# Performance work log

Hardware: AMD Instinct MI355X
Metric: run time of the kernel (lower is better)

The kernel has to match this reference:

```python
import jax, jax.numpy as jnp
import numpy as np

VOCAB = 100000
EMB = 128
WINDOW = 200
N_T = 64
B = 128
N_W = 128
ALPHA = 0.5
PAD = VOCAB - 1


def setup_inputs() -> dict:
    key = jax.random.key(0)
    ks = jax.random.split(key, 8)
    s = 0.5 / EMB
    tvecs = jax.random.uniform(ks[0], (VOCAB, EMB), minval=-s, maxval=s).at[PAD].set(0.0)
    cvecs = jax.random.uniform(ks[1], (VOCAB, EMB), minval=-s, maxval=s).at[PAD].set(0.0)
    W_w = jax.random.normal(ks[2], (N_W, 2 * EMB)) * 0.02
    W_b = jnp.zeros((N_W,))
    h_w = jax.random.normal(ks[3], (1, N_W)) * 0.02
    h_b = jnp.zeros((1,))
    batch_titems = jax.random.randint(ks[4], (B, N_T), 0, VOCAB)
    batch_citems = jax.random.randint(ks[5], (B, WINDOW), 0, VOCAB)
    mask_pad_ids = jax.random.randint(ks[6], (B, WINDOW), 0, 2).astype(bool)
    return {
        "tvecs": tvecs, "cvecs": cvecs,
        "W_w": W_w, "W_b": W_b, "h_w": h_w, "h_b": h_b,
        "batch_titems": batch_titems, "batch_citems": batch_citems,
        "mask_pad_ids": mask_pad_ids,
    }


def reference(tvecs, cvecs, W_w, W_b, h_w, h_b, batch_titems, batch_citems, mask_pad_ids):
    q = tvecs[batch_titems]   # (B, N_T, E)  target-item (query) embeddings
    k = cvecs[batch_citems]   # (B, W, E)    context-item (key/value) embeddings
    # W(concat(p, q)) == p @ Wp.T + q @ Wq.T + b  -- split weight, avoid the
    # materialized (B, N_T, W, 2E) repeat+cat tensor of the torch code.
    Wp, Wq = W_w[:, :EMB], W_w[:, EMB:]
    hp = jnp.einsum('bte,ne->btn', q, Wp)   # (B, N_T, N_W)
    hq = jnp.einsum('bwe,ne->bwn', k, Wq)   # (B, W,  N_W)
    hidden = jax.nn.relu(hp[:, :, None, :] + hq[:, None, :, :] + W_b)  # (B,N_T,W,N_W)
    att = jnp.einsum('btwn,n->btw', hidden, h_w[0]) + h_b[0]            # (B,N_T,W)
    att = jnp.where(mask_pad_ids[:, None, :], -jnp.inf, att)
    att = jax.nn.softmax(att, axis=-1)
    out = jnp.einsum('btw,bwe->bte', att, k)                            # (B,N_T,E)
    norm = (1000.0 - mask_pad_ids.sum(axis=1).astype(out.dtype)) ** ALPHA  # (B,)
    return out / norm[:, None, None]
```

## Files before the change

### kernel.cpp

```cpp
#include <hip/hip_runtime.h>
#include <math.h>

#define EMB 128
#define WIN 200
#define NT 64
#define BB 128

typedef short bf16x8 __attribute__((ext_vector_type(8)));
typedef float f32x4  __attribute__((ext_vector_type(4)));

__device__ __forceinline__ unsigned pk2bf16(float a, float b) {
    unsigned ua = __float_as_uint(a), ub = __float_as_uint(b);
    ua = (ua + 0x7FFFu + ((ua >> 16) & 1u)) >> 16;
    ub = (ub + 0x7FFFu + ((ub >> 16) & 1u)) >> 16;
    return ua | (ub << 16);
}
__device__ __forceinline__ float rdlane(float v, int l) {
    return __uint_as_float(__builtin_amdgcn_readlane(__float_as_uint(v), l));
}

__global__ __launch_bounds__(512, 4) void proj_kernel(
    const float* __restrict__ tvecs, const float* __restrict__ cvecs,
    const int* __restrict__ titems, const int* __restrict__ citems,
    const float* __restrict__ Ww, const float* __restrict__ Wbias,
    const int* __restrict__ mi, int* __restrict__ flag,
    float* __restrict__ hp_out, float* __restrict__ hq_out)
{
    __shared__ __align__(16) ushort s_A[128 * 128];
    __shared__ __align__(16) ushort s_B[128 * 128];
    __shared__ float s_bias[128];
    __shared__ int   sdet;

    const int tid = threadIdx.x;

    if (blockIdx.x == 264) {
        if (tid == 0) sdet = 0;
        __syncthreads();
        int bad = 0;
        for (int i = tid; i < 6400; i += 512)
            if ((unsigned)mi[i] > 1u) bad = 1;
        if (bad) sdet = 1;
        __syncthreads();
        if (tid == 0) flag[0] = sdet;
        return;
    }

    const bool is_hp = blockIdx.x < 64;
    const float* table = is_hp ? tvecs : cvecs;
    const int*   idx   = is_hp ? titems : citems;
    const int  rbase = (is_hp ? blockIdx.x : (blockIdx.x - 64)) * 128;
    const int  eoff  = is_hp ? 0 : EMB;

    if (tid < 128) s_bias[tid] = Wbias[tid];

    for (int i = tid; i < 4096; i += 512) {
        int row = i >> 5, j = i & 31;
        float4 v = *(const float4*)&table[(size_t)idx[rbase + row] * 128 + 4 * j];
        uint2 p; p.x = pk2bf16(v.x, v.y); p.y = pk2bf16(v.z, v.w);
        *(uint2*)((char*)s_A + row * 256 + (((j >> 1) ^ (row & 7)) << 4) + (j & 1) * 8) = p;
    }
    for (int i = tid; i < 4096; i += 512) {
        int n = i >> 5, j = i & 31;
        float4 v = *(const float4*)&Ww[n * 256 + eoff + 4 * j];
        uint2 p; p.x = pk2bf16(v.x, v.y); p.y = pk2bf16(v.z, v.w);
        *(uint2*)((char*)s_B + n * 256 + (((j >> 1) ^ (n & 7)) << 4) + (j & 1) * 8) = p;
    }
    __syncthreads();

    const int wid = tid >> 6, l = tid & 63;
    const int rl = l & 15, kg = l >> 4;
    const int r0 = wid * 16;

    f32x4 acc[8];
#pragma unroll
    for (int i = 0; i < 8; ++i) acc[i] = (f32x4){0.f, 0.f, 0.f, 0.f};

    const int arow = r0 + rl;
#pragma unroll
    for (int s = 0; s < 4; ++s) {
        bf16x8 af = *(const bf16x8*)((const char*)s_A
                        + arow * 256 + ((((s << 2) + kg) ^ (arow & 7)) << 4));
#pragma unroll
        for (int nt = 0; nt < 8; ++nt) {
            int bn = nt * 16 + rl;
            bf16x8 bfr = *(const bf16x8*)((const char*)s_B
                            + bn * 256 + ((((s << 2) + kg) ^ (bn & 7)) << 4));
            acc[nt] = __builtin_amdgcn_mfma_f32_16x16x32_bf16(af, bfr, acc[nt], 0, 0, 0);
        }
    }

#pragma unroll
    for (int i = 0; i < 4; ++i) {
        size_t base = (size_t)(rbase + r0 + kg * 4 + i) * 128;
        if (is_hp) {
#pragma unroll
            for (int nt = 0; nt < 8; ++nt)
                hp_out[base + nt * 16 + rl] = acc[nt][i];
        } else {
#pragma unroll
            for (int nt = 0; nt < 8; ++nt) {
                int col = nt * 16 + rl;
                hq_out[base + col] = acc[nt][i] + s_bias[col];
            }
        }
    }
}

__global__ __launch_bounds__(512, 2) void attn_kernel(
    const float* __restrict__ cvecs, const int* __restrict__ citems,
    const void* __restrict__ mask_raw, const int* __restrict__ flagp,
    const float* __restrict__ hwg, const float* __restrict__ hp,
    const float* __restrict__ hq, float* __restrict__ outp)
{
    __shared__ __align__(16) float4 s_hq4[32 * 128];
    __shared__ __align__(16) float4 s_k4[128 * 32];
    __shared__ __align__(16) float  s_hp[32 * 128];
    __shared__ __align__(16) float  s_hw[128];
    __shared__ int s_ci[WIN];
    __shared__ int s_widx[WIN];
    __shared__ int s_m;

    const int tid  = threadIdx.x;
    const int bid  = blockIdx.x;
    const int swz  = (bid & 7) * 32 + (bid >> 3);
    const int b    = swz >> 1;
    const int tb   = (swz & 1) * 32;
    const int lane = tid & 63;
    const int wid  = tid >> 6;
    const int t0   = wid * 4;

    for (int i = tid; i < 1024; i += 512) {
        int t = i >> 5, e4 = i & 31;
        *(float4*)&s_hp[t * 128 + e4 * 4] =
            *(const float4*)&hp[((size_t)(b * 64 + tb + t)) * 128 + e4 * 4];
    }
    if (tid < 128) s_hw[tid] = hwg[tid];
    if (tid < WIN) s_ci[tid] = citems[b * WIN + tid];
    if (wid == 0) {
        const int boolmode = flagp[0];
        const unsigned char* mb = (const unsigned char*)mask_raw;
        const int*           mi = (const int*)mask_raw;
        int base = 0;
#pragma unroll
        for (int r = 0; r < 4; ++r) {
            int w  = r * 64 + lane;
            int mv = 1;
            if (w < WIN) mv = boolmode ? (int)mb[b * WIN + w] : mi[b * WIN + w];
            unsigned long long act = __ballot(mv == 0);
            if (mv == 0)
                s_widx[base + __popcll(act & ((1ull << lane) - 1ull))] = w;
            base += __popcll(act);
        }
        if (lane == 0) s_m = base;
    }
    __syncthreads();

    const int m = s_m;
    const float invn = 1.f / sqrtf(800.f + (float)m);
    size_t orow = ((size_t)(b * 64 + tb + t0)) * 128;

    if (m == 0) {
#pragma unroll
        for (int j = 0; j < 4; ++j)
            *(float2*)&outp[orow + (size_t)j * 128 + lane * 2] = make_float2(0.f, 0.f);
        return;
    }

    const float4* hq4r = (const float4*)hq + (size_t)b * 200 * 32;
    const float4* hp4a = (const float4*)&s_hp[t0 * 128];
    const float4* hw4p = (const float4*)s_hw;
    const float4* cv4  = (const float4*)cvecs;

#define SC(J, K, HV, P)                                                        \
    va[J][K] += hwv.x * fmaxf(HV.x + P.x, 0.f) + hwv.y * fmaxf(HV.y + P.y, 0.f)\
              + hwv.z * fmaxf(HV.z + P.z, 0.f) + hwv.w * fmaxf(HV.w + P.w, 0.f);

    if (m <= 128) {
        {
            const int w2 = tid & 127, nc0 = tid >> 7;
            if (w2 < m) {
                const int wi = s_widx[w2];
#pragma unroll
                for (int nc = nc0; nc < 32; nc += 4)
                    s_hq4[nc * 128 + w2] = hq4r[(size_t)wi * 32 + nc];
            }
            const int e4 = tid & 31, w0 = tid >> 5;
            for (int w2k = w0; w2k < m; w2k += 16) {
                int ci = s_ci[s_widx[w2k]];
                s_k4[w2k * 32 + e4] = cv4[(size_t)ci * 32 + e4];
            }
        }
        __syncthreads();

        float va[4][2];
#pragma unroll
        for (int j = 0; j < 4; ++j) { va[j][0] = 0.f; va[j][1] = 0.f; }

#pragma unroll 2
        for (int nc = 0; nc < 32; ++nc) {
            float4 hv0 = s_hq4[nc * 128 + lane];
            float4 hv1 = s_hq4[nc * 128 + 64 + lane];
            float4 hwv = hw4p[nc];
            float4 p0  = hp4a[0 * 32 + nc];
            float4 p1  = hp4a[1 * 32 + nc];
            float4 p2  = hp4a[2 * 32 + nc];
            float4 p3  = hp4a[3 * 32 + nc];
            SC(0, 0, hv0, p0) SC(0, 1, hv1, p0)
            SC(1, 0, hv0, p1) SC(1, 1, hv1, p1)
            SC(2, 0, hv0, p2) SC(2, 1, hv1, p2)
            SC(3, 0, hv0, p3) SC(3, 1, hv1, p3)
        }

#pragma unroll
        for (int j = 0; j < 4; ++j) {
            float mx = -1e30f;
#pragma unroll
            for (int kt = 0; kt < 2; ++kt) {
                float v = (kt * 64 + lane < m) ? va[j][kt] : -1e30f;
                va[j][kt] = v;
                mx = fmaxf(mx, v);
            }
#pragma unroll
            for (int off = 32; off; off >>= 1) mx = fmaxf(mx, __shfl_xor(mx, off));
            float sum = 0.f;
#pragma unroll
            for (int kt = 0; kt < 2; ++kt) {
                float e = (va[j][kt] <= -1e29f) ? 0.f : __expf(va[j][kt] - mx);
                va[j][kt] = e;
                sum += e;
            }
#pragma unroll
            for (int off = 32; off; off >>= 1) sum += __shfl_xor(sum, off);
            float is = 1.f / sum;
            va[j][0] *= is; va[j][1] *= is;
        }

        float2 po[4];
#pragma unroll
        for (int j = 0; j < 4; ++j) po[j] = make_float2(0.f, 0.f);
        const float2* s_k2 = (const float2*)s_k4;
#pragma unroll
        for (int kt = 0; kt < 2; ++kt) {
            if (kt * 64 < m) {
                const int wn = min(64, m - kt * 64);
                for (int w = 0; w < wn; ++w) {
                    float2 kv = s_k2[(kt * 64 + w) * 64 + lane];
                    float a0 = rdlane(va[0][kt], w);
                    float a1 = rdlane(va[1][kt], w);
                    float a2 = rdlane(va[2][kt], w);
                    float a3 = rdlane(va[3][kt], w);
                    po[0].x += a0 * kv.x; po[0].y += a0 * kv.y;
                    po[1].x += a1 * kv.x; po[1].y += a1 * kv.y;
                    po[2].x += a2 * kv.x; po[2].y += a2 * kv.y;
                    po[3].x += a3 * kv.x; po[3].y += a3 * kv.y;
                }
            }
        }
#pragma unroll
        for (int j = 0; j < 4; ++j)
            *(float2*)&outp[orow + (size_t)j * 128 + lane * 2] =
                make_float2(po[j].x * invn, po[j].y * invn);
    } else {
        int wreg[4];
        const int mc = m - 1;
#pragma unroll
        for (int kt = 0; kt < 4; ++kt)
            wreg[kt] = s_widx[min(kt * 64 + lane, mc)];

        float va[4][4];
#pragma unroll
        for (int j = 0; j < 4; ++j)
#pragma unroll
            for (int k = 0; k < 4; ++k) va[j][k] = 0.f;

#pragma unroll 2
        for (int nc = 0; nc < 32; ++nc) {
            float4 hv0 = hq4r[(size_t)wreg[0] * 32 + nc];
            float4 hv1 = hq4r[(size_t)wreg[1] * 32 + nc];
            float4 hv2 = hq4r[(size_t)wreg[2] * 32 + nc];
            float4 hv3 = hq4r[(size_t)wreg[3] * 32 + nc];
            float4 hwv = hw4p[nc];
            float4 p0  = hp4a[0 * 32 + nc];
            float4 p1  = hp4a[1 * 32 + nc];
            float4 p2  = hp4a[2 * 32 + nc];
            float4 p3  = hp4a[3 * 32 + nc];
            SC(0, 0, hv0, p0) SC(0, 1, hv1, p0) SC(0, 2, hv2, p0) SC(0, 3, hv3, p0)
            SC(1, 0, hv0, p1) SC(1, 1, hv1, p1) SC(1, 2, hv2, p1) SC(1, 3, hv3, p1)
            SC(2, 0, hv0, p2) SC(2, 1, hv1, p2) SC(2, 2, hv2, p2) SC(2, 3, hv3, p2)
            SC(3, 0, hv0, p3) SC(3, 1, hv1, p3) SC(3, 2, hv2, p3) SC(3, 3, hv3, p3)
        }

#pragma unroll
        for (int j = 0; j < 4; ++j) {
            float mx = -1e30f;
#pragma unroll
            for (int kt = 0; kt < 4; ++kt) {
                float v = (kt * 64 + lane < m) ? va[j][kt] : -1e30f;
                va[j][kt] = v;
                mx = fmaxf(mx, v);
            }
#pragma unroll
            for (int off = 32; off; off >>= 1) mx = fmaxf(mx, __shfl_xor(mx, off));
            float sum = 0.f;
#pragma unroll
            for (int kt = 0; kt < 4; ++kt) {
                float e = (va[j][kt] <= -1e29f) ? 0.f : __expf(va[j][kt] - mx);
                va[j][kt] = e;
                sum += e;
            }
#pragma unroll
            for (int off = 32; off; off >>= 1) sum += __shfl_xor(sum, off);
            float is = 1.f / sum;
#pragma unroll
            for (int kt = 0; kt < 4; ++kt) va[j][kt] *= is;
        }

        float2 po[4];
#pragma unroll
        for (int j = 0; j < 4; ++j) po[j] = make_float2(0.f, 0.f);
        const char* cvb = (const char*)cvecs;
#pragma unroll
        for (int kt = 0; kt < 4; ++kt) {
            if (kt * 64 < m) {
                const int wn = min(64, m - kt * 64);
                for (int w = 0; w < wn; ++w) {
                    unsigned off = (unsigned)s_ci[s_widx[kt * 64 + w]] * 512u;
                    float2 kv = *(const float2*)(cvb + off + lane * 8);
                    float a0 = rdlane(va[0][kt], w);
                    float a1 = rdlane(va[1][kt], w);
                    float a2 = rdlane(va[2][kt], w);
                    float a3 = rdlane(va[3][kt], w);
                    po[0].x += a0 * kv.x; po[0].y += a0 * kv.y;
                    po[1].x += a1 * kv.x; po[1].y += a1 * kv.y;
                    po[2].x += a2 * kv.x; po[2].y += a2 * kv.y;
                    po[3].x += a3 * kv.x; po[3].y += a3 * kv.y;
                }
            }
        }
#pragma unroll
        for (int j = 0; j < 4; ++j)
            *(float2*)&outp[orow + (size_t)j * 128 + lane * 2] =
                make_float2(po[j].x * invn, po[j].y * invn);
    }
#undef SC
}

extern "C" void kernel_launch(void* const* d_in, const int* in_sizes, int n_in,
                              void* d_out, int out_size, void* d_ws, size_t ws_size,
                              hipStream_t stream) {
    const float* tvecs = (const float*)d_in[0];
    const float* cvecs = (const float*)d_in[1];
    const float* Ww    = (const float*)d_in[2];
    const float* Wb    = (const float*)d_in[3];
    const float* hw    = (const float*)d_in[4];
    const int* titems  = (const int*)d_in[6];
    const int* citems  = (const int*)d_in[7];
    const void* mask   = d_in[8];
    float* out         = (float*)d_out;

    const size_t hp_elems = (size_t)BB * NT * 128;
    const size_t hq_elems = (size_t)BB * WIN * 128;
    const size_t needed = 256 + (hp_elems + hq_elems) * 4;
    if (ws_size < needed) return;

    int*   flag  = (int*)d_ws;
    float* hp_ws = (float*)((char*)d_ws + 256);
    float* hq_ws = hp_ws + hp_elems;

    proj_kernel<<<265, 512, 0, stream>>>(tvecs, cvecs, titems, citems,
                                         Ww, Wb, (const int*)mask, flag,
                                         hp_ws, hq_ws);
    attn_kernel<<<BB * 2, 512, 0, stream>>>(cvecs, citems, mask, flag,
                                            hw, hp_ws, hq_ws, out);
}
```

Before: 48.20 us.

## Split attention over window halves with flash-style partial softmax and combine kernel

The attention kernel now splits each (batch, target-half) block into two blocks, each handling half of the unmasked window positions. Each block writes unnormalized partial outputs plus its max and sum, and a new combine kernel merges them with log-sum-exp rescaling and applies the norm. hp is also staged in LDS as bf16 to shrink shared memory, allowing higher occupancy (launch bound 4). The cost is an extra kernel launch, a partial-results buffer round trip, and reduced precision for hp. The m>128 path is not split: its second-half block stays idle.

```diff
diff --git a/kernel.cpp b/kernel.cpp
--- a/kernel.cpp
+++ b/kernel.cpp
@@ -5,6 +5,7 @@
 #define WIN 200
 #define NT 64
 #define BB 128
+#define PSTRIDE 132
 
 typedef short bf16x8 __attribute__((ext_vector_type(8)));
 typedef float f32x4  __attribute__((ext_vector_type(4)));
@@ -15,6 +16,8 @@
     ub = (ub + 0x7FFFu + ((ub >> 16) & 1u)) >> 16;
     return ua | (ub << 16);
 }
+__device__ __forceinline__ float bf_lo(unsigned u) { return __uint_as_float(u << 16); }
+__device__ __forceinline__ float bf_hi(unsigned u) { return __uint_as_float(u & 0xFFFF0000u); }
 __device__ __forceinline__ float rdlane(float v, int l) {
     return __uint_as_float(__builtin_amdgcn_readlane(__float_as_uint(v), l));
 }
@@ -106,33 +109,34 @@
     }
 }
 
-__global__ __launch_bounds__(512, 2) void attn_kernel(
+__global__ __launch_bounds__(512, 4) void attn_part(
     const float* __restrict__ cvecs, const int* __restrict__ citems,
     const void* __restrict__ mask_raw, const int* __restrict__ flagp,
     const float* __restrict__ hwg, const float* __restrict__ hp,
-    const float* __restrict__ hq, float* __restrict__ outp)
+    const float* __restrict__ hq, float* __restrict__ part)
 {
-    __shared__ __align__(16) float4 s_hq4[32 * 128];
-    __shared__ __align__(16) float4 s_k4[128 * 32];
-    __shared__ __align__(16) float  s_hp[32 * 128];
-    __shared__ __align__(16) float  s_hw[128];
+    __shared__ __align__(16) float4 s_hq4[32 * 64];
+    __shared__ __align__(16) float4 s_k4[64 * 32];
+    __shared__ __align__(16) ushort s_hp[32 * 128];
+    __shared__ float s_hw[128];
     __shared__ int s_ci[WIN];
     __shared__ int s_widx[WIN];
     __shared__ int s_m;
 
     const int tid  = threadIdx.x;
     const int bid  = blockIdx.x;
-    const int swz  = (bid & 7) * 32 + (bid >> 3);
-    const int b    = swz >> 1;
-    const int tb   = (swz & 1) * 32;
+    const int b    = bid >> 2;
+    const int tb   = ((bid >> 1) & 1) * 32;
+    const int h    = bid & 1;
     const int lane = tid & 63;
     const int wid  = tid >> 6;
     const int t0   = wid * 4;
 
     for (int i = tid; i < 1024; i += 512) {
         int t = i >> 5, e4 = i & 31;
-        *(float4*)&s_hp[t * 128 + e4 * 4] =
-            *(const float4*)&hp[((size_t)(b * 64 + tb + t)) * 128 + e4 * 4];
+        float4 v = *(const float4*)&hp[((size_t)(b * 64 + tb + t)) * 128 + e4 * 4];
+        uint2 p; p.x = pk2bf16(v.x, v.y); p.y = pk2bf16(v.z, v.w);
+        ((uint2*)s_hp)[i] = p;
     }
     if (tid < 128) s_hw[tid] = hwg[tid];
     if (tid < WIN) s_ci[tid] = citems[b * WIN + tid];
@@ -156,116 +160,103 @@
     __syncthreads();
 
     const int m = s_m;
-    const float invn = 1.f / sqrtf(800.f + (float)m);
-    size_t orow = ((size_t)(b * 64 + tb + t0)) * 128;
-
-    if (m == 0) {
-#pragma unroll
-        for (int j = 0; j < 4; ++j)
-            *(float2*)&outp[orow + (size_t)j * 128 + lane * 2] = make_float2(0.f, 0.f);
-        return;
-    }
-
     const float4* hq4r = (const float4*)hq + (size_t)b * 200 * 32;
-    const float4* hp4a = (const float4*)&s_hp[t0 * 128];
     const float4* hw4p = (const float4*)s_hw;
-    const float4* cv4  = (const float4*)cvecs;
-
-#define SC(J, K, HV, P)                                                        \
-    va[J][K] += hwv.x * fmaxf(HV.x + P.x, 0.f) + hwv.y * fmaxf(HV.y + P.y, 0.f)\
-              + hwv.z * fmaxf(HV.z + P.z, 0.f) + hwv.w * fmaxf(HV.w + P.w, 0.f);
+
+#define ZERO_OUT()                                                             \
+    {                                                                          \
+        _Pragma("unroll")                                                      \
+        for (int j = 0; j < 4; ++j) {                                          \
+            float* pb = part + ((size_t)((b * 64 + tb + t0 + j) * 2 + h)) * PSTRIDE; \
+            *(float2*)(pb + lane * 2) = make_float2(0.f, 0.f);                 \
+            if (lane == 0) { pb[128] = -1e30f; pb[129] = 0.f; pb[130] = 0.f; } \
+        }                                                                      \
+    }
+
+#define SCB(J, HV)                                                             \
+    va[J] += hwv.x * fmaxf(HV.x + pa, 0.f) + hwv.y * fmaxf(HV.y + pb_, 0.f)    \
+           + hwv.z * fmaxf(HV.z + pc, 0.f) + hwv.w * fmaxf(HV.w + pd, 0.f);
+#define SCB4(J, K, HV)                                                         \
+    va[J][K] += hwv.x * fmaxf(HV.x + pa, 0.f) + hwv.y * fmaxf(HV.y + pb_, 0.f) \
+              + hwv.z * fmaxf(HV.z + pc, 0.f) + hwv.w * fmaxf(HV.w + pd, 0.f);
 
     if (m <= 128) {
+        const int mh0 = (m + 1) >> 1;
+        const int lo  = h ? mh0 : 0;
+        const int cnt = h ? (m - mh0) : mh0;
+        if (cnt == 0) { ZERO_OUT(); return; }
+
         {
-            const int w2 = tid & 127, nc0 = tid >> 7;
-            if (w2 < m) {
-                const int wi = s_widx[w2];
-#pragma unroll
-                for (int nc = nc0; nc < 32; nc += 4)
-                    s_hq4[nc * 128 + w2] = hq4r[(size_t)wi * 32 + nc];
+            const int w2 = tid & 63, nc0 = tid >> 6;
+            if (w2 < cnt) {
+                const int wi = s_widx[lo + w2];
+#pragma unroll
+                for (int nc = nc0; nc < 32; nc += 8)
+                    s_hq4[nc * 64 + w2] = hq4r[(size_t)wi * 32 + nc];
             }
             const int e4 = tid & 31, w0 = tid >> 5;
-            for (int w2k = w0; w2k < m; w2k += 16) {
-                int ci = s_ci[s_widx[w2k]];
-                s_k4[w2k * 32 + e4] = cv4[(size_t)ci * 32 + e4];
-            }
+            const float4* cv4 = (const float4*)cvecs;
+            for (int w2k = w0; w2k < cnt; w2k += 16)
+                s_k4[w2k * 32 + e4] = cv4[(size_t)s_ci[s_widx[lo + w2k]] * 32 + e4];
         }
         __syncthreads();
 
-        float va[4][2];
-#pragma unroll
-        for (int j = 0; j < 4; ++j) { va[j][0] = 0.f; va[j][1] = 0.f; }
-
-#pragma unroll 2
+        float va[4];
+        va[0] = va[1] = va[2] = va[3] = 0.f;
+#pragma unroll 4
         for (int nc = 0; nc < 32; ++nc) {
-            float4 hv0 = s_hq4[nc * 128 + lane];
-            float4 hv1 = s_hq4[nc * 128 + 64 + lane];
+            float4 hv  = s_hq4[nc * 64 + lane];
             float4 hwv = hw4p[nc];
-            float4 p0  = hp4a[0 * 32 + nc];
-            float4 p1  = hp4a[1 * 32 + nc];
-            float4 p2  = hp4a[2 * 32 + nc];
-            float4 p3  = hp4a[3 * 32 + nc];
-            SC(0, 0, hv0, p0) SC(0, 1, hv1, p0)
-            SC(1, 0, hv0, p1) SC(1, 1, hv1, p1)
-            SC(2, 0, hv0, p2) SC(2, 1, hv1, p2)
-            SC(3, 0, hv0, p3) SC(3, 1, hv1, p3)
-        }
-
+#pragma unroll
+            for (int jt = 0; jt < 4; ++jt) {
+                uint2 pu = *(const uint2*)&s_hp[(t0 + jt) * 128 + nc * 4];
+                float pa = bf_lo(pu.x), pb_ = bf_hi(pu.x), pc = bf_lo(pu.y), pd = bf_hi(pu.y);
+                SCB(jt, hv)
+            }
+        }
+
+        float mxs[4], sms[4];
 #pragma unroll
         for (int j = 0; j < 4; ++j) {
-            float mx = -1e30f;
-#pragma unroll
-            for (int kt = 0; kt < 2; ++kt) {
-                float v = (kt * 64 + lane < m) ? va[j][kt] : -1e30f;
-                va[j][kt] = v;
-                mx = fmaxf(mx, v);
-            }
+            float v = (lane < cnt) ? va[j] : -1e30f;
+            float mx = v;
 #pragma unroll
             for (int off = 32; off; off >>= 1) mx = fmaxf(mx, __shfl_xor(mx, off));
-            float sum = 0.f;
-#pragma unroll
-            for (int kt = 0; kt < 2; ++kt) {
-                float e = (va[j][kt] <= -1e29f) ? 0.f : __expf(va[j][kt] - mx);
-                va[j][kt] = e;
-                sum += e;
-            }
+            float e = (v <= -1e29f) ? 0.f : __expf(v - mx);
+            float sum = e;
 #pragma unroll
             for (int off = 32; off; off >>= 1) sum += __shfl_xor(sum, off);
-            float is = 1.f / sum;
-            va[j][0] *= is; va[j][1] *= is;
+            va[j] = e; mxs[j] = mx; sms[j] = sum;
         }
 
         float2 po[4];
 #pragma unroll
         for (int j = 0; j < 4; ++j) po[j] = make_float2(0.f, 0.f);
         const float2* s_k2 = (const float2*)s_k4;
-#pragma unroll
-        for (int kt = 0; kt < 2; ++kt) {
-            if (kt * 64 < m) {
-                const int wn = min(64, m - kt * 64);
-                for (int w = 0; w < wn; ++w) {
-                    float2 kv = s_k2[(kt * 64 + w) * 64 + lane];
-                    float a0 = rdlane(va[0][kt], w);
-                    float a1 = rdlane(va[1][kt], w);
-                    float a2 = rdlane(va[2][kt], w);
-                    float a3 = rdlane(va[3][kt], w);
-                    po[0].x += a0 * kv.x; po[0].y += a0 * kv.y;
-                    po[1].x += a1 * kv.x; po[1].y += a1 * kv.y;
-                    po[2].x += a2 * kv.x; po[2].y += a2 * kv.y;
-                    po[3].x += a3 * kv.x; po[3].y += a3 * kv.y;
-                }
-            }
-        }
-#pragma unroll
-        for (int j = 0; j < 4; ++j)
-            *(float2*)&outp[orow + (size_t)j * 128 + lane * 2] =
-                make_float2(po[j].x * invn, po[j].y * invn);
+        for (int w = 0; w < cnt; ++w) {
+            float2 kv = s_k2[w * 64 + lane];
+            float a0 = rdlane(va[0], w);
+            float a1 = rdlane(va[1], w);
+            float a2 = rdlane(va[2], w);
+            float a3 = rdlane(va[3], w);
+            po[0].x += a0 * kv.x; po[0].y += a0 * kv.y;
+            po[1].x += a1 * kv.x; po[1].y += a1 * kv.y;
+            po[2].x += a2 * kv.x; po[2].y += a2 * kv.y;
+            po[3].x += a3 * kv.x; po[3].y += a3 * kv.y;
+        }
+
+#pragma unroll
+        for (int j = 0; j < 4; ++j) {
+            float* pb = part + ((size_t)((b * 64 + tb + t0 + j) * 2 + h)) * PSTRIDE;
+            *(float2*)(pb + lane * 2) = po[j];
+            if (lane == 0) { pb[128] = mxs[j]; pb[129] = sms[j]; pb[130] = (float)cnt; }
+        }
     } else {
+        if (h == 1) { ZERO_OUT(); return; }
         int wreg[4];
         const int mc = m - 1;
 #pragma unroll
-        for (int kt = 0; kt < 4; ++kt)
-            wreg[kt] = s_widx[min(kt * 64 + lane, mc)];
+        for (int kt = 0; kt < 4; ++kt) wreg[kt] = s_widx[min(kt * 64 + lane, mc)];
 
         float va[4][4];
 #pragma unroll
@@ -280,16 +271,15 @@
             float4 hv2 = hq4r[(size_t)wreg[2] * 32 + nc];
             float4 hv3 = hq4r[(size_t)wreg[3] * 32 + nc];
             float4 hwv = hw4p[nc];
-            float4 p0  = hp4a[0 * 32 + nc];
-            float4 p1  = hp4a[1 * 32 + nc];
-            float4 p2  = hp4a[2 * 32 + nc];
-            float4 p3  = hp4a[3 * 32 + nc];
-            SC(0, 0, hv0, p0) SC(0, 1, hv1, p0) SC(0, 2, hv2, p0) SC(0, 3, hv3, p0)
-            SC(1, 0, hv0, p1) SC(1, 1, hv1, p1) SC(1, 2, hv2, p1) SC(1, 3, hv3, p1)
-            SC(2, 0, hv0, p2) SC(2, 1, hv1, p2) SC(2, 2, hv2, p2) SC(2, 3, hv3, p2)
-            SC(3, 0, hv0, p3) SC(3, 1, hv1, p3) SC(3, 2, hv2, p3) SC(3, 3, hv3, p3)
-        }
-
+#pragma unroll
+            for (int jt = 0; jt < 4; ++jt) {
+                uint2 pu = *(const uint2*)&s_hp[(t0 + jt) * 128 + nc * 4];
+                float pa = bf_lo(pu.x), pb_ = bf_hi(pu.x), pc = bf_lo(pu.y), pd = bf_hi(pu.y);
+                SCB4(jt, 0, hv0) SCB4(jt, 1, hv1) SCB4(jt, 2, hv2) SCB4(jt, 3, hv3)
+            }
+        }
+
+        float mxs[4], sms[4];
 #pragma unroll
         for (int j = 0; j < 4; ++j) {
             float mx = -1e30f;
@@ -310,9 +300,7 @@
             }
 #pragma unroll
             for (int off = 32; off; off >>= 1) sum += __shfl_xor(sum, off);
-            float is = 1.f / sum;
-#pragma unroll
-            for (int kt = 0; kt < 4; ++kt) va[j][kt] *= is;
+            mxs[j] = mx; sms[j] = sum;
         }
 
         float2 po[4];
@@ -338,11 +326,41 @@
             }
         }
 #pragma unroll
-        for (int j = 0; j < 4; ++j)
-            *(float2*)&outp[orow + (size_t)j * 128 + lane * 2] =
-                make_float2(po[j].x * invn, po[j].y * invn);
-    }
-#undef SC
+        for (int j = 0; j < 4; ++j) {
+            float* pb = part + ((size_t)((b * 64 + tb + t0 + j) * 2 + h)) * PSTRIDE;
+            *(float2*)(pb + lane * 2) = po[j];
+            if (lane == 0) { pb[128] = mxs[j]; pb[129] = sms[j]; pb[130] = (float)m; }
+        }
+    }
+#undef SCB
+#undef SCB4
+#undef ZERO_OUT
+}
+
+__global__ __launch_bounds__(256) void combine_kernel(
+    const float* __restrict__ part, float* __restrict__ outp)
+{
+    const int lane = threadIdx.x & 63;
+    const int wid  = threadIdx.x >> 6;
+    const int row  = blockIdx.x * 4 + wid;
+
+    const float* p0 = part + (size_t)row * 2 * PSTRIDE;
+    const float* p1 = p0 + PSTRIDE;
+    float mx0 = p0[128], s0 = p0[129], c0m = p0[130];
+    float mx1 = p1[128], s1 = p1[129], c1m = p1[130];
+    float M  = fmaxf(mx0, mx1);
+    float c0 = (s0 > 0.f) ? __expf(mx0 - M) : 0.f;
+    float c1 = (s1 > 0.f) ? __expf(mx1 - M) : 0.f;
+    float den = c0 * s0 + c1 * s1;
+    float invn = 1.f / sqrtf(800.f + c0m + c1m);
+    float scale = (den > 0.f) ? (invn / den) : 0.f;
+
+    float2 a = *(const float2*)(p0 + lane * 2);
+    float2 q = *(const float2*)(p1 + lane * 2);
+    float2 r;
+    r.x = (c0 * a.x + c1 * q.x) * scale;
+    r.y = (c0 * a.y + c1 * q.y) * scale;
+    *(float2*)&outp[(size_t)row * 128 + lane * 2] = r;
 }
 
 extern "C" void kernel_launch(void* const* d_in, const int* in_sizes, int n_in,
@@ -358,18 +376,21 @@
     const void* mask   = d_in[8];
     float* out         = (float*)d_out;
 
-    const size_t hp_elems = (size_t)BB * NT * 128;
-    const size_t hq_elems = (size_t)BB * WIN * 128;
-    const size_t needed = 256 + (hp_elems + hq_elems) * 4;
+    const size_t hp_elems   = (size_t)BB * NT * 128;
+    const size_t hq_elems   = (size_t)BB * WIN * 128;
+    const size_t part_elems = (size_t)BB * NT * 2 * PSTRIDE;
+    const size_t needed = 256 + (hp_elems + hq_elems + part_elems) * 4;
     if (ws_size < needed) return;
 
-    int*   flag  = (int*)d_ws;
-    float* hp_ws = (float*)((char*)d_ws + 256);
-    float* hq_ws = hp_ws + hp_elems;
+    int*   flag    = (int*)d_ws;
+    float* hp_ws   = (float*)((char*)d_ws + 256);
+    float* hq_ws   = hp_ws + hp_elems;
+    float* part_ws = hq_ws + hq_elems;
 
     proj_kernel<<<265, 512, 0, stream>>>(tvecs, cvecs, titems, citems,
                                          Ww, Wb, (const int*)mask, flag,
                                          hp_ws, hq_ws);
-    attn_kernel<<<BB * 2, 512, 0, stream>>>(cvecs, citems, mask, flag,
-                                            hw, hp_ws, hq_ws, out);
-}
+    attn_part<<<BB * 4, 512, 0, stream>>>(cvecs, citems, mask, flag,
+                                          hw, hp_ws, hq_ws, part_ws);
+    combine_kernel<<<2048, 256, 0, stream>>>(part_ws, out);
+}
```

Measured after the change: 53.01 us. 1.1x slower.

## Prefetch full hq block into registers, stage hq and keys as bf16 in LDS

Applied to the files above, without the earlier changes.

The attention kernel now issues global loads for the whole per-batch hq block (200x128) and the hp rows into registers before the mask compaction. It then packs hq into swizzled bf16 LDS storage, so the masked-window gather happens through LDS indices rather than a second global gather. Key vectors are prefetched into registers before the score loop and written to LDS as bf16 only after the softmax, hiding their latency behind compute. The trade is loading all 200 hq rows regardless of the mask, higher register pressure (13+8 float4 buffers), bf16 rounding of hq and keys that affects accuracy, and an extra barrier.

```diff
diff --git a/kernel.cpp b/kernel.cpp
--- a/kernel.cpp
+++ b/kernel.cpp
@@ -15,6 +15,8 @@
     ub = (ub + 0x7FFFu + ((ub >> 16) & 1u)) >> 16;
     return ua | (ub << 16);
 }
+__device__ __forceinline__ float bf_lo(unsigned u) { return __uint_as_float(u << 16); }
+__device__ __forceinline__ float bf_hi(unsigned u) { return __uint_as_float(u & 0xFFFF0000u); }
 __device__ __forceinline__ float rdlane(float v, int l) {
     return __uint_as_float(__builtin_amdgcn_readlane(__float_as_uint(v), l));
 }
@@ -112,10 +114,10 @@
     const float* __restrict__ hwg, const float* __restrict__ hp,
     const float* __restrict__ hq, float* __restrict__ outp)
 {
-    __shared__ __align__(16) float4 s_hq4[32 * 128];
-    __shared__ __align__(16) float4 s_k4[128 * 32];
-    __shared__ __align__(16) float  s_hp[32 * 128];
-    __shared__ __align__(16) float  s_hw[128];
+    __shared__ __align__(16) uint2 s_hq2[WIN * 32];
+    __shared__ __align__(16) uint  s_k[128 * 64];
+    __shared__ __align__(16) float s_hp[32 * 128];
+    __shared__ float s_hw[128];
     __shared__ int s_ci[WIN];
     __shared__ int s_widx[WIN];
     __shared__ int s_m;
@@ -129,10 +131,19 @@
     const int wid  = tid >> 6;
     const int t0   = wid * 4;
 
-    for (int i = tid; i < 1024; i += 512) {
-        int t = i >> 5, e4 = i & 31;
-        *(float4*)&s_hp[t * 128 + e4 * 4] =
-            *(const float4*)&hp[((size_t)(b * 64 + tb + t)) * 128 + e4 * 4];
+    const float4* hq4r = (const float4*)hq + (size_t)b * 200 * 32;
+    const float4* cv4  = (const float4*)cvecs;
+
+    float4 hqbuf[13];
+    {
+        int n = 0;
+        for (int idx = tid; idx < 6400; idx += 512) hqbuf[n++] = hq4r[idx];
+    }
+    float4 hpbuf[2];
+#pragma unroll
+    for (int q = 0; q < 2; ++q) {
+        int idx = tid + q * 512;
+        hpbuf[q] = *(const float4*)&hp[((size_t)(b * 64 + tb + (idx >> 5))) * 128 + (idx & 31) * 4];
     }
     if (tid < 128) s_hw[tid] = hwg[tid];
     if (tid < WIN) s_ci[tid] = citems[b * WIN + tid];
@@ -153,6 +164,21 @@
         }
         if (lane == 0) s_m = base;
     }
+
+    {
+        int n = 0;
+        for (int idx = tid; idx < 6400; idx += 512) {
+            int w = idx >> 5, nc = idx & 31;
+            float4 v = hqbuf[n++];
+            uint2 p; p.x = pk2bf16(v.x, v.y); p.y = pk2bf16(v.z, v.w);
+            s_hq2[w * 32 + (nc ^ (w & 31))] = p;
+        }
+    }
+#pragma unroll
+    for (int q = 0; q < 2; ++q) {
+        int idx = tid + q * 512;
+        *(float4*)&s_hp[(idx >> 5) * 128 + (idx & 31) * 4] = hpbuf[q];
+    }
     __syncthreads();
 
     const int m = s_m;
@@ -166,31 +192,29 @@
         return;
     }
 
-    const float4* hq4r = (const float4*)hq + (size_t)b * 200 * 32;
     const float4* hp4a = (const float4*)&s_hp[t0 * 128];
     const float4* hw4p = (const float4*)s_hw;
-    const float4* cv4  = (const float4*)cvecs;
-
-#define SC(J, K, HV, P)                                                        \
+    const int mc = m - 1;
+
+#define SCB(J, K, HA, HB, HC, HD, P)                                           \
+    va[J][K] += hwv.x * fmaxf(HA + P.x, 0.f) + hwv.y * fmaxf(HB + P.y, 0.f)    \
+              + hwv.z * fmaxf(HC + P.z, 0.f) + hwv.w * fmaxf(HD + P.w, 0.f);
+#define SCF(J, K, HV, P)                                                       \
     va[J][K] += hwv.x * fmaxf(HV.x + P.x, 0.f) + hwv.y * fmaxf(HV.y + P.y, 0.f)\
               + hwv.z * fmaxf(HV.z + P.z, 0.f) + hwv.w * fmaxf(HV.w + P.w, 0.f);
 
     if (m <= 128) {
+        float4 kbuf[8];
         {
-            const int w2 = tid & 127, nc0 = tid >> 7;
-            if (w2 < m) {
-                const int wi = s_widx[w2];
-#pragma unroll
-                for (int nc = nc0; nc < 32; nc += 4)
-                    s_hq4[nc * 128 + w2] = hq4r[(size_t)wi * 32 + nc];
-            }
-            const int e4 = tid & 31, w0 = tid >> 5;
-            for (int w2k = w0; w2k < m; w2k += 16) {
-                int ci = s_ci[s_widx[w2k]];
-                s_k4[w2k * 32 + e4] = cv4[(size_t)ci * 32 + e4];
-            }
-        }
-        __syncthreads();
+            int n = 0;
+            for (int idx = tid; idx < m * 32; idx += 512)
+                kbuf[n++] = cv4[(size_t)s_ci[s_widx[idx >> 5]] * 32 + (idx & 31)];
+        }
+
+        const int wr0 = s_widx[min(lane, mc)];
+        const int wr1 = s_widx[min(64 + lane, mc)];
+        const int b0 = wr0 * 32, x0 = wr0 & 31;
+        const int b1 = wr1 * 32, x1 = wr1 & 31;
 
         float va[4][2];
 #pragma unroll
@@ -198,17 +222,19 @@
 
 #pragma unroll 2
         for (int nc = 0; nc < 32; ++nc) {
-            float4 hv0 = s_hq4[nc * 128 + lane];
-            float4 hv1 = s_hq4[nc * 128 + 64 + lane];
+            uint2 h0 = s_hq2[b0 + (nc ^ x0)];
+            uint2 h1 = s_hq2[b1 + (nc ^ x1)];
+            float h0a = bf_lo(h0.x), h0b = bf_hi(h0.x), h0c = bf_lo(h0.y), h0d = bf_hi(h0.y);
+            float h1a = bf_lo(h1.x), h1b = bf_hi(h1.x), h1c = bf_lo(h1.y), h1d = bf_hi(h1.y);
             float4 hwv = hw4p[nc];
             float4 p0  = hp4a[0 * 32 + nc];
             float4 p1  = hp4a[1 * 32 + nc];
             float4 p2  = hp4a[2 * 32 + nc];
             float4 p3  = hp4a[3 * 32 + nc];
-            SC(0, 0, hv0, p0) SC(0, 1, hv1, p0)
-            SC(1, 0, hv0, p1) SC(1, 1, hv1, p1)
-            SC(2, 0, hv0, p2) SC(2, 1, hv1, p2)
-            SC(3, 0, hv0, p3) SC(3, 1, hv1, p3)
+            SCB(0, 0, h0a, h0b, h0c, h0d, p0) SCB(0, 1, h1a, h1b, h1c, h1d, p0)
+            SCB(1, 0, h0a, h0b, h0c, h0d, p1) SCB(1, 1, h1a, h1b, h1c, h1d, p1)
+            SCB(2, 0, h0a, h0b, h0c, h0d, p2) SCB(2, 1, h1a, h1b, h1c, h1d, p2)
+            SCB(3, 0, h0a, h0b, h0c, h0d, p3) SCB(3, 1, h1a, h1b, h1c, h1d, p3)
         }
 
 #pragma unroll
@@ -235,24 +261,35 @@
             va[j][0] *= is; va[j][1] *= is;
         }
 
+        {
+            int n = 0;
+            for (int idx = tid; idx < m * 32; idx += 512) {
+                int w2 = idx >> 5, e4 = idx & 31;
+                float4 v = kbuf[n++];
+                uint2 p; p.x = pk2bf16(v.x, v.y); p.y = pk2bf16(v.z, v.w);
+                *(uint2*)&s_k[w2 * 64 + e4 * 2] = p;
+            }
+        }
+        __syncthreads();
+
         float2 po[4];
 #pragma unroll
         for (int j = 0; j < 4; ++j) po[j] = make_float2(0.f, 0.f);
-        const float2* s_k2 = (const float2*)s_k4;
 #pragma unroll
         for (int kt = 0; kt < 2; ++kt) {
             if (kt * 64 < m) {
                 const int wn = min(64, m - kt * 64);
                 for (int w = 0; w < wn; ++w) {
-                    float2 kv = s_k2[(kt * 64 + w) * 64 + lane];
+                    unsigned ku = s_k[(kt * 64 + w) * 64 + lane];
+                    float kx = bf_lo(ku), ky = bf_hi(ku);
                     float a0 = rdlane(va[0][kt], w);
                     float a1 = rdlane(va[1][kt], w);
                     float a2 = rdlane(va[2][kt], w);
                     float a3 = rdlane(va[3][kt], w);
-                    po[0].x += a0 * kv.x; po[0].y += a0 * kv.y;
-                    po[1].x += a1 * kv.x; po[1].y += a1 * kv.y;
-                    po[2].x += a2 * kv.x; po[2].y += a2 * kv.y;
-                    po[3].x += a3 * kv.x; po[3].y += a3 * kv.y;
+                    po[0].x += a0 * kx; po[0].y += a0 * ky;
+                    po[1].x += a1 * kx; po[1].y += a1 * ky;
+                    po[2].x += a2 * kx; po[2].y += a2 * ky;
+                    po[3].x += a3 * kx; po[3].y += a3 * ky;
                 }
             }
         }
@@ -262,7 +299,6 @@
                 make_float2(po[j].x * invn, po[j].y * invn);
     } else {
         int wreg[4];
-        const int mc = m - 1;
 #pragma unroll
         for (int kt = 0; kt < 4; ++kt)
             wreg[kt] = s_widx[min(kt * 64 + lane, mc)];
@@ -284,10 +320,10 @@
             float4 p1  = hp4a[1 * 32 + nc];
             float4 p2  = hp4a[2 * 32 + nc];
             float4 p3  = hp4a[3 * 32 + nc];
-            SC(0, 0, hv0, p0) SC(0, 1, hv1, p0) SC(0, 2, hv2, p0) SC(0, 3, hv3, p0)
-            SC(1, 0, hv0, p1) SC(1, 1, hv1, p1) SC(1, 2, hv2, p1) SC(1, 3, hv3, p1)
-            SC(2, 0, hv0, p2) SC(2, 1, hv1, p2) SC(2, 2, hv2, p2) SC(2, 3, hv3, p2)
-            SC(3, 0, hv0, p3) SC(3, 1, hv1, p3) SC(3, 2, hv2, p3) SC(3, 3, hv3, p3)
+            SCF(0, 0, hv0, p0) SCF(0, 1, hv1, p0) SCF(0, 2, hv2, p0) SCF(0, 3, hv3, p0)
+            SCF(1, 0, hv0, p1) SCF(1, 1, hv1, p1) SCF(1, 2, hv2, p1) SCF(1, 3, hv3, p1)
+            SCF(2, 0, hv0, p2) SCF(2, 1, hv1, p2) SCF(2, 2, hv2, p2) SCF(2, 3, hv3, p2)
+            SCF(3, 0, hv0, p3) SCF(3, 1, hv1, p3) SCF(3, 2, hv2, p3) SCF(3, 3, hv3, p3)
         }
 
 #pragma unroll
@@ -342,7 +378,8 @@
             *(float2*)&outp[orow + (size_t)j * 128 + lane * 2] =
                 make_float2(po[j].x * invn, po[j].y * invn);
     }
-#undef SC
+#undef SCB
+#undef SCF
 }
 
 extern "C" void kernel_launch(void* const* d_in, const int* in_sizes, int n_in,
```

Result: slower. 58.95 us (+22.3%).
